# Kernel tuning notes

Hardware: AMD Instinct MI355X
Metric: run time of the kernel (lower is better)

Reference implementation:

```python
import jax, jax.numpy as jnp
import numpy as np

N = 50000   # active sparse voxels
B = 4       # batch size
FIN = 64
FOUT = 128
TEMB = 256
K = 27      # 3x3x3 kernel offsets
EPS = 1e-5


def _bn(x, gamma, beta, mean, var):
    # inference-style BatchNorm over channel dim
    return (x - mean) * jax.lax.rsqrt(var + EPS) * gamma + beta


def _sparse_conv(feats, nbr, mask, W):
    # submanifold sparse conv via kernel map:
    # out[n] = sum_k mask[k,n] * feats[nbr[k,n]] @ W[k]
    g = feats[nbr] * mask[..., None].astype(feats.dtype)   # [K, N, Fin]
    return jnp.einsum('knf,kfo->no', g, W)                  # [N, Fout]


def _make_kernel_map(k_nbr, k_msk, n):
    nbr = jax.random.randint(k_nbr, (K, N), 0, n, dtype=jnp.int32)
    mask = jax.random.bernoulli(k_msk, 0.4, (K, N))
    # center offset is the identity map and always valid (submanifold conv)
    nbr = nbr.at[K // 2].set(jnp.arange(N, dtype=jnp.int32))
    mask = mask.at[K // 2].set(True)
    return nbr, mask


def setup_inputs() -> dict:
    key = jax.random.key(0)
    ks = jax.random.split(key, 20)
    x_feats = jax.random.normal(ks[0], (N, FIN), jnp.float32)
    batch_idx = jax.random.randint(ks[1], (N,), 0, B, dtype=jnp.int32)
    t = jax.random.normal(ks[2], (B, TEMB), jnp.float32)
    nbr1, mask1 = _make_kernel_map(ks[3], ks[4], N)
    nbr2, mask2 = _make_kernel_map(ks[5], ks[6], N)
    s1 = 1.0 / np.sqrt(FIN * K)
    s2 = 1.0 / np.sqrt(FOUT * K)
    return {
        'x_feats': x_feats, 'batch_idx': batch_idx, 't': t,
        'nbr1': nbr1, 'mask1': mask1, 'nbr2': nbr2, 'mask2': mask2,
        'bn1_gamma': jnp.ones((FIN,), jnp.float32),
        'bn1_beta': jnp.zeros((FIN,), jnp.float32),
        'bn1_mean': 0.1 * jax.random.normal(ks[7], (FIN,), jnp.float32),
        'bn1_var': jax.random.uniform(ks[8], (FIN,), jnp.float32, 0.5, 1.5),
        'W1': s1 * jax.random.normal(ks[9], (K, FIN, FOUT), jnp.float32),
        't_W': (1.0 / np.sqrt(TEMB)) * jax.random.normal(ks[10], (TEMB, FOUT), jnp.float32),
        't_b': jnp.zeros((FOUT,), jnp.float32),
        'bn2_gamma': jnp.ones((FOUT,), jnp.float32),
        'bn2_beta': jnp.zeros((FOUT,), jnp.float32),
        'bn2_mean': 0.1 * jax.random.normal(ks[11], (FOUT,), jnp.float32),
        'bn2_var': jax.random.uniform(ks[12], (FOUT,), jnp.float32, 0.5, 1.5),
        'W2': s2 * jax.random.normal(ks[13], (K, FOUT, FOUT), jnp.float32),
        'res_W': (1.0 / np.sqrt(FIN)) * jax.random.normal(ks[14], (FIN, FOUT), jnp.float32),
        'res_b': jnp.zeros((FOUT,), jnp.float32),
    }


def reference(x_feats, batch_idx, t, nbr1, mask1, nbr2, mask2,
              bn1_gamma, bn1_beta, bn1_mean, bn1_var, W1,
              t_W, t_b,
              bn2_gamma, bn2_beta, bn2_mean, bn2_var, W2,
              res_W, res_b):
    # conv1 block: BN -> SiLU -> sparse Conv3d
    h = jax.nn.silu(_bn(x_feats, bn1_gamma, bn1_beta, bn1_mean, bn1_var))
    h = _sparse_conv(h, nbr1, mask1, W1)                      # [N, FOUT]
    # FiLM-style time embedding, broadcast per point via batch index
    t_emb = jax.nn.silu(t) @ t_W + t_b                        # [B, FOUT]
    h = h + t_emb[batch_idx]
    # conv2 block
    h2 = jax.nn.silu(_bn(h, bn2_gamma, bn2_beta, bn2_mean, bn2_var))
    h2 = _sparse_conv(h2, nbr2, mask2, W2)                    # [N, FOUT]
    # residual connection (f_in != f_out -> Linear)
    return h2 + (x_feats @ res_W + res_b)
```

## Files before the change

### kernel.cpp

```cpp
#include <hip/hip_runtime.h>


#define EPS 1e-5f

typedef __attribute__((ext_vector_type(8))) short s16x8;
typedef __attribute__((ext_vector_type(4))) float f32x4;
typedef __attribute__((ext_vector_type(4))) unsigned short u16x4;

#define VPB 98

static __device__ __forceinline__ unsigned short f2bf(float f) {
    union { float f; unsigned u; } v; v.f = f;
    unsigned r = v.u + 0x7fffu + ((v.u >> 16) & 1u);
    return (unsigned short)(r >> 16);
}
static __device__ __forceinline__ float silu_d(float x) {
    return x / (1.f + __expf(-x));
}
static __device__ __forceinline__ void gload_lds16(const void* gsrc, void* ldst) {
    __builtin_amdgcn_global_load_lds(
        (const __attribute__((address_space(1))) unsigned int*)gsrc,
        (__attribute__((address_space(3))) unsigned int*)ldst, 16, 0, 0);
}
static __device__ __forceinline__ int mask_shift(const unsigned char* mask, int NV) {
    size_t base = (size_t)13 * (size_t)NV;
    int v = ((base & 3) == 3) ? 2 : 1;
    return (mask[base + v] == 1) ? 0 : 2;
}

#define NSH 2624
__global__ __launch_bounds__(256) void k_prep_fused(
        const float* __restrict__ t, const float* __restrict__ tW,
        const float* __restrict__ tb,
        const float* __restrict__ g2, const float* __restrict__ b2,
        const float* __restrict__ m2, const float* __restrict__ v2,
        float* __restrict__ temb, float* __restrict__ sc, float* __restrict__ sh,
        const float* __restrict__ W1, const float* __restrict__ W2,
        const float* __restrict__ rW,
        unsigned short* __restrict__ W1s, unsigned short* __restrict__ W2s,
        unsigned short* __restrict__ rWs,
        const float* __restrict__ x,
        const float* __restrict__ g1, const float* __restrict__ b1,
        const float* __restrict__ m1, const float* __restrict__ v1,
        unsigned short* __restrict__ h1, int NV, int B) {
    const int bid = blockIdx.x;
    if (bid < 2) {
        int idx = bid * 256 + threadIdx.x;
        if (idx < B * 128) {
            int b = idx >> 7, o = idx & 127;
            float s = 0.f;
            for (int e = 0; e < 256; ++e) {
                float tv = t[b * 256 + e];
                s += silu_d(tv) * tW[e * 128 + o];
            }
            temb[idx] = s + tb[o];
        }
        return;
    }
    if (bid == 2) {
        int tid = threadIdx.x;
        if (tid < 128) {
            float rstd = rsqrtf(v2[tid] + EPS);
            float s1 = g2[tid] * rstd;
            sc[tid] = s1;
            sh[tid] = b2[tid] - m2[tid] * s1;
        }
        return;
    }
    if (bid < 3 + NSH) {
        int tid = (bid - 3) * 256 + threadIdx.x;
        const int n1 = 432 * 512, n2 = 864 * 512, n3 = 16 * 512;
        if (tid < n1) {
            int f = tid >> 9, r = tid & 511, lane = r >> 3, j = r & 7;
            int mt = f & 7, fk = f >> 3, ks = fk & 1, ko = fk >> 1;
            int fin = ks * 32 + (lane >> 4) * 8 + j;
            int fout = mt * 16 + (lane & 15);
            W1s[tid] = f2bf(W1[(ko * 64 + fin) * 128 + fout]);
        } else if (tid < n1 + n2) {
            int e = tid - n1;
            int f = e >> 9, r = e & 511, lane = r >> 3, j = r & 7;
            int mt = f & 7, fk = f >> 3, ks = fk & 3, ko = fk >> 2;
            int fin = ks * 32 + (lane >> 4) * 8 + j;
            int fout = mt * 16 + (lane & 15);
            W2s[e] = f2bf(W2[(ko * 128 + fin) * 128 + fout]);
        } else if (tid < n1 + n2 + n3) {
            int e = tid - n1 - n2;
            int f = e >> 9, r = e & 511, lane = r >> 3, j = r & 7;
            int mt = f & 7, ks = f >> 3;
            int fin = ks * 32 + (lane >> 4) * 8 + j;
            int fout = mt * 16 + (lane & 15);
            rWs[e] = f2bf(rW[fin * 128 + fout]);
        }
        return;
    }
    {
        int tid = (bid - 3 - NSH) * 256 + threadIdx.x;
        if (tid >= NV * 16) return;
        int n = tid >> 4, c = (tid & 15) << 2;
        f32x4 xv = *(const f32x4*)(x + n * 64 + c);
        f32x4 gv = *(const f32x4*)(g1 + c);
        f32x4 bv = *(const f32x4*)(b1 + c);
        f32x4 mv = *(const f32x4*)(m1 + c);
        f32x4 vv = *(const f32x4*)(v1 + c);
        u16x4 ho;
#pragma unroll
        for (int j = 0; j < 4; ++j) {
            float xn = (xv[j] - mv[j]) * rsqrtf(vv[j] + EPS) * gv[j] + bv[j];
            ho[j] = f2bf(silu_d(xn));
        }
        *(u16x4*)(h1 + n * 64 + c) = ho;
    }
}

__global__ __launch_bounds__(448) void k_conv1(
        const unsigned short* __restrict__ h1, const int* __restrict__ nbr,
        const unsigned char* __restrict__ mask, const unsigned short* __restrict__ W1s,
        const float* __restrict__ temb, const int* __restrict__ bidx,
        const float* __restrict__ bn2sc, const float* __restrict__ bn2sh,
        unsigned short* __restrict__ h2in, int NV) {
    __shared__ unsigned short lds0[8192];
    __shared__ unsigned short lds1[8192];
    const int lane = threadIdx.x & 63;
    const int wave = threadIdx.x >> 6;
    const int g = lane >> 4, col = lane & 15;
    const int slot = wave * 16 + col;
    const int v = blockIdx.x * VPB + slot;
    const bool vok = (slot < VPB) && (v < NV);
    const int msh = mask_shift(mask, NV);

    f32x4 acc[8];
    const f32x4 z4 = {0.f, 0.f, 0.f, 0.f};
#pragma unroll
    for (int m = 0; m < 8; ++m) acc[m] = z4;
    const s16x8 zz = {0, 0, 0, 0, 0, 0, 0, 0};

    auto loadr = [&](int t) -> int {
        if (!vok) return -1;
        int off = t * NV + v;
        int nv = nbr[off];
        bool mm = mask[(size_t)off << msh] != 0;
        return mm ? nv : -1;
    };

    for (int off = threadIdx.x * 16; off < 16384; off += 7168)
        gload_lds16((const char*)W1s + off, (char*)lds0 + off);
    int rA = loadr(0);
    int rN = loadr(1);
    int r0 = rA < 0 ? 0 : rA;
    s16x8 p0 = *(const s16x8*)(h1 + r0 * 64 + 0 * 32 + g * 8);
    s16x8 p1 = *(const s16x8*)(h1 + r0 * 64 + 1 * 32 + g * 8);
    __syncthreads();

    unsigned short* bufc = lds0;
    unsigned short* bufn = lds1;

    for (int t = 0; t < 27; ++t) {
        s16x8 q0, q1;
        int rN2 = -1;
        if (t < 26) {
            const char* src = (const char*)W1s + (size_t)(t + 1) * 16384;
            for (int off = threadIdx.x * 16; off < 16384; off += 7168)
                gload_lds16(src + off, (char*)bufn + off);
            int rn = rN < 0 ? 0 : rN;
            q0 = *(const s16x8*)(h1 + rn * 64 + 0 * 32 + g * 8);
            q1 = *(const s16x8*)(h1 + rn * 64 + 1 * 32 + g * 8);
        }
        if (t < 25) rN2 = loadr(t + 2);
        const bool m = rA >= 0;
        s16x8 b0 = m ? p0 : zz;
        s16x8 b1 = m ? p1 : zz;
        const unsigned short* wp = bufc + lane * 8;
#pragma unroll
        for (int mt = 0; mt < 8; ++mt) {
            s16x8 a = *(const s16x8*)(wp + (0 * 8 + mt) * 512);
            acc[mt] = __builtin_amdgcn_mfma_f32_16x16x32_bf16(a, b0, acc[mt], 0, 0, 0);
        }
#pragma unroll
        for (int mt = 0; mt < 8; ++mt) {
            s16x8 a = *(const s16x8*)(wp + (1 * 8 + mt) * 512);
            acc[mt] = __builtin_amdgcn_mfma_f32_16x16x32_bf16(a, b1, acc[mt], 0, 0, 0);
        }
        if (t < 26) {
            __syncthreads();
            p0 = q0; p1 = q1;
            rA = rN; rN = rN2;
            unsigned short* tmp = bufc; bufc = bufn; bufn = tmp;
        }
    }

    if (vok) {
        int b = bidx[v];
        const float* te = temb + b * 128;
#pragma unroll
        for (int mt = 0; mt < 8; ++mt) {
            int c = mt * 16 + g * 4;
            f32x4 val = acc[mt];
            f32x4 tv = *(const f32x4*)(te + c);
            f32x4 sc = *(const f32x4*)(bn2sc + c);
            f32x4 sh = *(const f32x4*)(bn2sh + c);
            u16x4 o;
#pragma unroll
            for (int j = 0; j < 4; ++j) {
                float zv = (val[j] + tv[j]) * sc[j] + sh[j];
                o[j] = f2bf(silu_d(zv));
            }
            *(u16x4*)(h2in + v * 128 + c) = o;
        }
    }
}

__global__ __launch_bounds__(448) void k_conv2(
        const unsigned short* __restrict__ h2in, const int* __restrict__ nbr,
        const unsigned char* __restrict__ mask, const unsigned short* __restrict__ W2s,
        const float* __restrict__ x, const unsigned short* __restrict__ rWs,
        const float* __restrict__ resb, float* __restrict__ out, int NV) {
    __shared__ unsigned short lds0[16384];
    __shared__ unsigned short lds1[16384];
    const int lane = threadIdx.x & 63;
    const int wave = threadIdx.x >> 6;
    const int g = lane >> 4, col = lane & 15;
    const int slot = wave * 16 + col;
    const int v = blockIdx.x * VPB + slot;
    const bool vok = (slot < VPB) && (v < NV);
    const int msh = mask_shift(mask, NV);

    f32x4 acc[8];
    const f32x4 z4 = {0.f, 0.f, 0.f, 0.f};
#pragma unroll
    for (int m = 0; m < 8; ++m) acc[m] = z4;
    const s16x8 zz = {0, 0, 0, 0, 0, 0, 0, 0};

    auto loadr = [&](int t) -> int {
        if (!vok) return -1;
        int off = t * NV + v;
        int nv = nbr[off];
        bool mm = mask[(size_t)off << msh] != 0;
        return mm ? nv : -1;
    };

    for (int off = threadIdx.x * 16; off < 32768; off += 7168)
        gload_lds16((const char*)W2s + off, (char*)lds0 + off);
    int rA = loadr(0);
    int rN = loadr(1);
    int r0 = rA < 0 ? 0 : rA;
    s16x8 p0 = *(const s16x8*)(h2in + r0 * 128 + 0 * 32 + g * 8);
    s16x8 p1 = *(const s16x8*)(h2in + r0 * 128 + 1 * 32 + g * 8);
    s16x8 p2 = *(const s16x8*)(h2in + r0 * 128 + 2 * 32 + g * 8);
    s16x8 p3 = *(const s16x8*)(h2in + r0 * 128 + 3 * 32 + g * 8);

    {
        int rv = vok ? v : 0;
#pragma unroll
        for (int ks = 0; ks < 2; ++ks) {
            f32x4 xa = *(const f32x4*)(x + rv * 64 + ks * 32 + g * 8);
            f32x4 xb = *(const f32x4*)(x + rv * 64 + ks * 32 + g * 8 + 4);
            s16x8 b;
#pragma unroll
            for (int j = 0; j < 4; ++j) {
                b[j]     = (short)f2bf(xa[j]);
                b[j + 4] = (short)f2bf(xb[j]);
            }
            const unsigned short* wp = rWs + ks * 4096 + lane * 8;
#pragma unroll
            for (int mt = 0; mt < 8; ++mt) {
                s16x8 a = *(const s16x8*)(wp + mt * 512);
                acc[mt] = __builtin_amdgcn_mfma_f32_16x16x32_bf16(a, b, acc[mt], 0, 0, 0);
            }
        }
    }
    __syncthreads();

    unsigned short* bufc = lds0;
    unsigned short* bufn = lds1;

    for (int t = 0; t < 27; ++t) {
        s16x8 q0, q1, q2, q3;
        int rN2 = -1;
        if (t < 26) {
            const char* src = (const char*)W2s + (size_t)(t + 1) * 32768;
            for (int off = threadIdx.x * 16; off < 32768; off += 7168)
                gload_lds16(src + off, (char*)bufn + off);
            int rn = rN < 0 ? 0 : rN;
            q0 = *(const s16x8*)(h2in + rn * 128 + 0 * 32 + g * 8);
            q1 = *(const s16x8*)(h2in + rn * 128 + 1 * 32 + g * 8);
            q2 = *(const s16x8*)(h2in + rn * 128 + 2 * 32 + g * 8);
            q3 = *(const s16x8*)(h2in + rn * 128 + 3 * 32 + g * 8);
        }
        if (t < 25) rN2 = loadr(t + 2);
        const bool m = rA >= 0;
        s16x8 b0 = m ? p0 : zz;
        s16x8 b1 = m ? p1 : zz;
        s16x8 b2 = m ? p2 : zz;
        s16x8 b3 = m ? p3 : zz;
        const unsigned short* wp = bufc + lane * 8;
#pragma unroll
        for (int mt = 0; mt < 8; ++mt) {
            s16x8 a = *(const s16x8*)(wp + (0 * 8 + mt) * 512);
            acc[mt] = __builtin_amdgcn_mfma_f32_16x16x32_bf16(a, b0, acc[mt], 0, 0, 0);
        }
#pragma unroll
        for (int mt = 0; mt < 8; ++mt) {
            s16x8 a = *(const s16x8*)(wp + (1 * 8 + mt) * 512);
            acc[mt] = __builtin_amdgcn_mfma_f32_16x16x32_bf16(a, b1, acc[mt], 0, 0, 0);
        }
#pragma unroll
        for (int mt = 0; mt < 8; ++mt) {
            s16x8 a = *(const s16x8*)(wp + (2 * 8 + mt) * 512);
            acc[mt] = __builtin_amdgcn_mfma_f32_16x16x32_bf16(a, b2, acc[mt], 0, 0, 0);
        }
#pragma unroll
        for (int mt = 0; mt < 8; ++mt) {
            s16x8 a = *(const s16x8*)(wp + (3 * 8 + mt) * 512);
            acc[mt] = __builtin_amdgcn_mfma_f32_16x16x32_bf16(a, b3, acc[mt], 0, 0, 0);
        }
        if (t < 26) {
            __syncthreads();
            p0 = q0; p1 = q1; p2 = q2; p3 = q3;
            rA = rN; rN = rN2;
            unsigned short* tmp = bufc; bufc = bufn; bufn = tmp;
        }
    }

    if (vok) {
#pragma unroll
        for (int mt = 0; mt < 8; ++mt) {
            int c = mt * 16 + g * 4;
            f32x4 rr = acc[mt] + *(const f32x4*)(resb + c);
            *(f32x4*)(out + v * 128 + c) = rr;
        }
    }
}

extern "C" void kernel_launch(void* const* d_in, const int* in_sizes, int n_in,
                              void* d_out, int out_size, void* d_ws, size_t ws_size,
                              hipStream_t stream) {
    const float* x          = (const float*)d_in[0];
    const int* bidx         = (const int*)d_in[1];
    const float* t          = (const float*)d_in[2];
    const int* nbr1         = (const int*)d_in[3];
    const unsigned char* mask1 = (const unsigned char*)d_in[4];
    const int* nbr2         = (const int*)d_in[5];
    const unsigned char* mask2 = (const unsigned char*)d_in[6];
    const float* bn1g       = (const float*)d_in[7];
    const float* bn1b       = (const float*)d_in[8];
    const float* bn1m       = (const float*)d_in[9];
    const float* bn1v       = (const float*)d_in[10];
    const float* W1         = (const float*)d_in[11];
    const float* tW         = (const float*)d_in[12];
    const float* tb         = (const float*)d_in[13];
    const float* bn2g       = (const float*)d_in[14];
    const float* bn2b       = (const float*)d_in[15];
    const float* bn2m       = (const float*)d_in[16];
    const float* bn2v       = (const float*)d_in[17];
    const float* W2         = (const float*)d_in[18];
    const float* rW         = (const float*)d_in[19];
    const float* resb       = (const float*)d_in[20];

    const int NV = in_sizes[0] / 64;
    const int B  = in_sizes[2] / 256;
    float* out = (float*)d_out;

    char* ws = (char*)d_ws;
    size_t o_W1s = 0;
    size_t o_W2s = o_W1s + (size_t)432 * 1024;
    size_t o_rWs = o_W2s + (size_t)864 * 1024;
    size_t o_te  = o_rWs + (size_t)16 * 1024;
    size_t o_sc  = o_te  + (size_t)B * 128 * 4;
    size_t o_sh  = o_sc  + 512;
    size_t o_h1  = o_sh  + 512;
    size_t o_h2  = o_h1  + (size_t)NV * 64 * 2;

    unsigned short* W1s  = (unsigned short*)(ws + o_W1s);
    unsigned short* W2s  = (unsigned short*)(ws + o_W2s);
    unsigned short* rWs  = (unsigned short*)(ws + o_rWs);
    float* temb  = (float*)(ws + o_te);
    float* bn2sc = (float*)(ws + o_sc);
    float* bn2sh = (float*)(ws + o_sh);
    unsigned short* h1   = (unsigned short*)(ws + o_h1);
    unsigned short* h2in = (unsigned short*)(ws + o_h2);

    {
        int nel = (NV * 16 + 255) / 256;
        int grid = 3 + NSH + nel;
        k_prep_fused<<<grid, 256, 0, stream>>>(
            t, tW, tb, bn2g, bn2b, bn2m, bn2v, temb, bn2sc, bn2sh,
            W1, W2, rW, W1s, W2s, rWs,
            x, bn1g, bn1b, bn1m, bn1v, h1, NV, B);
    }
    {
        int grid = (NV + VPB - 1) / VPB;
        k_conv1<<<grid, 448, 0, stream>>>(h1, nbr1, mask1, W1s, temb, bidx,
                                          bn2sc, bn2sh, h2in, NV);
        k_conv2<<<grid, 448, 0, stream>>>(h2in, nbr2, mask2, W2s, x, rWs,
                                          resb, out, NV);
    }
}
```

Before: 122.4 us.

## Process two kernel offsets per pipeline stage in conv1

```diff
diff --git a/kernel.cpp b/kernel.cpp
--- a/kernel.cpp
+++ b/kernel.cpp
@@ -118,8 +118,8 @@
         const float* __restrict__ temb, const int* __restrict__ bidx,
         const float* __restrict__ bn2sc, const float* __restrict__ bn2sh,
         unsigned short* __restrict__ h2in, int NV) {
-    __shared__ unsigned short lds0[8192];
-    __shared__ unsigned short lds1[8192];
+    __shared__ unsigned short lds0[16384];
+    __shared__ unsigned short lds1[16384];
     const int lane = threadIdx.x & 63;
     const int wave = threadIdx.x >> 6;
     const int g = lane >> 4, col = lane & 15;
@@ -135,55 +135,77 @@
     const s16x8 zz = {0, 0, 0, 0, 0, 0, 0, 0};
 
     auto loadr = [&](int t) -> int {
-        if (!vok) return -1;
+        if (!vok || t >= 27) return -1;
         int off = t * NV + v;
         int nv = nbr[off];
         bool mm = mask[(size_t)off << msh] != 0;
         return mm ? nv : -1;
     };
 
-    for (int off = threadIdx.x * 16; off < 16384; off += 7168)
+    for (int off = threadIdx.x * 16; off < 32768; off += 7168)
         gload_lds16((const char*)W1s + off, (char*)lds0 + off);
-    int rA = loadr(0);
-    int rN = loadr(1);
-    int r0 = rA < 0 ? 0 : rA;
-    s16x8 p0 = *(const s16x8*)(h1 + r0 * 64 + 0 * 32 + g * 8);
-    s16x8 p1 = *(const s16x8*)(h1 + r0 * 64 + 1 * 32 + g * 8);
+    int ra = loadr(0), rb = loadr(1), rc = loadr(2), rd = loadr(3);
+    {
+        int r0 = ra < 0 ? 0 : ra;
+        int r1 = rb < 0 ? 0 : rb;
+    }
+    int r0i = ra < 0 ? 0 : ra;
+    int r1i = rb < 0 ? 0 : rb;
+    s16x8 pA0 = *(const s16x8*)(h1 + r0i * 64 + 0 * 32 + g * 8);
+    s16x8 pA1 = *(const s16x8*)(h1 + r0i * 64 + 1 * 32 + g * 8);
+    s16x8 pB0 = *(const s16x8*)(h1 + r1i * 64 + 0 * 32 + g * 8);
+    s16x8 pB1 = *(const s16x8*)(h1 + r1i * 64 + 1 * 32 + g * 8);
     __syncthreads();
 
     unsigned short* bufc = lds0;
     unsigned short* bufn = lds1;
 
-    for (int t = 0; t < 27; ++t) {
-        s16x8 q0, q1;
-        int rN2 = -1;
-        if (t < 26) {
-            const char* src = (const char*)W1s + (size_t)(t + 1) * 16384;
-            for (int off = threadIdx.x * 16; off < 16384; off += 7168)
+    for (int p = 0; p < 14; ++p) {
+        s16x8 qA0, qA1, qB0, qB1;
+        int re = -1, rf = -1;
+        if (p < 13) {
+            const char* src = (const char*)W1s + (size_t)(p + 1) * 32768;
+            for (int off = threadIdx.x * 16; off < 32768; off += 7168)
                 gload_lds16(src + off, (char*)bufn + off);
-            int rn = rN < 0 ? 0 : rN;
-            q0 = *(const s16x8*)(h1 + rn * 64 + 0 * 32 + g * 8);
-            q1 = *(const s16x8*)(h1 + rn * 64 + 1 * 32 + g * 8);
-        }
-        if (t < 25) rN2 = loadr(t + 2);
-        const bool m = rA >= 0;
-        s16x8 b0 = m ? p0 : zz;
-        s16x8 b1 = m ? p1 : zz;
+            int rn0 = rc < 0 ? 0 : rc;
+            int rn1 = rd < 0 ? 0 : rd;
+            qA0 = *(const s16x8*)(h1 + rn0 * 64 + 0 * 32 + g * 8);
+            qA1 = *(const s16x8*)(h1 + rn0 * 64 + 1 * 32 + g * 8);
+            qB0 = *(const s16x8*)(h1 + rn1 * 64 + 0 * 32 + g * 8);
+            qB1 = *(const s16x8*)(h1 + rn1 * 64 + 1 * 32 + g * 8);
+            re = loadr(2 * p + 4);
+            rf = loadr(2 * p + 5);
+        }
+        const bool ma = ra >= 0, mb = rb >= 0;
+        s16x8 a0 = ma ? pA0 : zz;
+        s16x8 a1 = ma ? pA1 : zz;
+        s16x8 b0 = mb ? pB0 : zz;
+        s16x8 b1 = mb ? pB1 : zz;
         const unsigned short* wp = bufc + lane * 8;
 #pragma unroll
         for (int mt = 0; mt < 8; ++mt) {
             s16x8 a = *(const s16x8*)(wp + (0 * 8 + mt) * 512);
+            acc[mt] = __builtin_amdgcn_mfma_f32_16x16x32_bf16(a, a0, acc[mt], 0, 0, 0);
+        }
+#pragma unroll
+        for (int mt = 0; mt < 8; ++mt) {
+            s16x8 a = *(const s16x8*)(wp + (1 * 8 + mt) * 512);
+            acc[mt] = __builtin_amdgcn_mfma_f32_16x16x32_bf16(a, a1, acc[mt], 0, 0, 0);
+        }
+#pragma unroll
+        for (int mt = 0; mt < 8; ++mt) {
+            s16x8 a = *(const s16x8*)(wp + (2 * 8 + mt) * 512);
             acc[mt] = __builtin_amdgcn_mfma_f32_16x16x32_bf16(a, b0, acc[mt], 0, 0, 0);
         }
 #pragma unroll
         for (int mt = 0; mt < 8; ++mt) {
-            s16x8 a = *(const s16x8*)(wp + (1 * 8 + mt) * 512);
+            s16x8 a = *(const s16x8*)(wp + (3 * 8 + mt) * 512);
             acc[mt] = __builtin_amdgcn_mfma_f32_16x16x32_bf16(a, b1, acc[mt], 0, 0, 0);
         }
-        if (t < 26) {
+        if (p < 13) {
             __syncthreads();
-            p0 = q0; p1 = q1;
-            rA = rN; rN = rN2;
+            pA0 = qA0; pA1 = qA1; pB0 = qB0; pB1 = qB1;
+            ra = rc; rb = rd; rc = re; rd = rf;
             unsigned short* tmp = bufc; bufc = bufn; bufn = tmp;
         }
     }
@@ -362,7 +384,7 @@
 
     char* ws = (char*)d_ws;
     size_t o_W1s = 0;
-    size_t o_W2s = o_W1s + (size_t)432 * 1024;
+    size_t o_W2s = o_W1s + (size_t)448 * 1024;
     size_t o_rWs = o_W2s + (size_t)864 * 1024;
     size_t o_te  = o_rWs + (size_t)16 * 1024;
     size_t o_sc  = o_te  + (size_t)B * 128 * 4;
```

Measured after the change: 127.0 us. +3.8%, slower.
